# Kernel optimization log

Measured on AMD Instinct MI355X. Metric: run time of the kernel, lower is better.

## Reference

```python
import jax, jax.numpy as jnp
import numpy as np

B, N, S, K, D = 4, 8192, 2048, 32, 64
RADIUS = 0.2
MLP = [64, 64, 128]
C_IN = 3 + D  # 67
EPS = 1e-5  # BatchNorm eps


def setup_inputs() -> dict:
    key = jax.random.key(0)
    ks = jax.random.split(key, 8)
    inp = {
        "xyz": jax.random.uniform(ks[0], (B, N, 3), dtype=jnp.float32),
        "points": jax.random.normal(ks[1], (B, N, D), dtype=jnp.float32) * 0.1,
    }
    c = C_IN
    for i, o in enumerate(MLP):
        inp[f"w{i}"] = jax.random.normal(ks[2 + i], (o, c), dtype=jnp.float32) / np.sqrt(c).astype(np.float32)
        inp[f"b{i}"] = jnp.zeros((o,), jnp.float32)
        inp[f"g{i}"] = jnp.ones((o,), jnp.float32)
        inp[f"be{i}"] = jnp.zeros((o,), jnp.float32)
        c = o
    return inp


def _farthest_point_sample(xyz, npoint):
    # xyz: [B,N,3] -> idx [B,npoint]. Deterministic start at index 0
    # (torch version uses a random start index).
    Bb, Nn, _ = xyz.shape

    def step(carry, _):
        dist, far = carry
        centroid = jnp.take_along_axis(xyz, far[:, None, None], axis=1)  # [B,1,3]
        d = jnp.sum((xyz - centroid) ** 2, axis=-1)  # [B,N]
        dist = jnp.minimum(dist, d)
        nxt = jnp.argmax(dist, axis=-1).astype(jnp.int32)
        return (dist, nxt), far

    init = (jnp.full((Bb, Nn), 1e18, xyz.dtype), jnp.zeros((Bb,), jnp.int32))
    _, idx = jax.lax.scan(step, init, None, length=npoint)  # [npoint,B]
    return idx.T


def _square_distance(src, dst):
    # src [B,S,3], dst [B,N,3] -> [B,S,N]
    d = -2.0 * jnp.einsum("bsc,bnc->bsn", src, dst)
    d = d + jnp.sum(src ** 2, -1)[:, :, None] + jnp.sum(dst ** 2, -1)[:, None, :]
    return jnp.maximum(d, 0.0)


def _query_ball_point(radius, nsample, xyz, new_xyz):
    Bb, Nn, _ = xyz.shape
    sqr = _square_distance(new_xyz, xyz)  # [B,S,N]
    gi = jnp.broadcast_to(jnp.arange(Nn, dtype=jnp.int32), sqr.shape)
    gi = jnp.where(sqr > radius ** 2, Nn, gi)
    gi = jnp.sort(gi, axis=-1)[..., :nsample]  # [B,S,nsample]
    first = gi[..., :1]
    gi = jnp.where(gi >= Nn, first, gi)
    return jnp.clip(gi, 0, Nn - 1)


def _forward(xyz, points, params):
    bidx = jnp.arange(B)[:, None]
    fps_idx = _farthest_point_sample(xyz, S)          # [B,S]
    new_xyz = xyz[bidx, fps_idx]                      # [B,S,3]
    idx = _query_ball_point(RADIUS, K, xyz, new_xyz)  # [B,S,K]
    bidx3 = jnp.arange(B)[:, None, None]
    grouped_xyz = xyz[bidx3, idx]                     # [B,S,K,3]
    gnorm = grouped_xyz - new_xyz[:, :, None, :]
    gpts = points[bidx3, idx]                         # [B,S,K,D]
    feat = jnp.concatenate([gnorm, gpts], axis=-1)    # [B,S,K,3+D]
    x = jnp.transpose(feat, (0, 3, 2, 1))             # [B,C,K,S]
    for (w, b, g, be) in params:
        x = jnp.einsum("oc,bcks->boks", w, x) + b[None, :, None, None]
        mu = jnp.mean(x, axis=(0, 2, 3), keepdims=True)     # BN training mode
        var = jnp.var(x, axis=(0, 2, 3), keepdims=True)
        x = g[None, :, None, None] * (x - mu) * jax.lax.rsqrt(var + EPS) + be[None, :, None, None]
        x = jax.nn.relu(x)
    new_points = jnp.max(x, axis=2)                   # [B,mlp[-1],S]
    return new_xyz, new_points


def reference(xyz, points, w0, b0, g0, be0, w1, b1, g1, be1, w2, b2, g2, be2):
    params = ((w0, b0, g0, be0), (w1, b1, g1, be1), (w2, b2, g2, be2))
    return _forward(xyz, points, params)
```

## Files before the change

### kernel.cpp

```cpp
#include <hip/hip_runtime.h>
#include <hip/hip_bf16.h>

#define BB 4
#define NN 8192
#define SS 2048
#define KK 32
#define DD 64
#define CIN 67
#define PPIX (BB*SS*KK)
#define CNT_F 262144.0f
#define R2 0.04f
#define BN_EPS 1e-5f

typedef unsigned long long ull;

__global__ void zero_kernel(float* __restrict__ p, int n) {
    int i = blockIdx.x * 256 + threadIdx.x;
    if (i < n) p[i] = 0.0f;
}

__global__ __launch_bounds__(512) void fps_kernel(const float* __restrict__ xyz,
                                                  float* __restrict__ out_newxyz) {
    const int b = blockIdx.x;
    const int t = threadIdx.x;
    const int w = t >> 6, lane = t & 63;
    const float* X = xyz + (size_t)b * NN * 3;

    float px[16], py[16], pz[16], dist[16];
#pragma unroll
    for (int j = 0; j < 16; j++) {
        int i = t * 16 + j;
        px[j] = X[3 * i];
        py[j] = X[3 * i + 1];
        pz[j] = X[3 * i + 2];
        dist[j] = 1e18f;
    }

    __shared__ ull sSlot[2][8];

    float cx = X[0], cy = X[1], cz = X[2];

    for (int s = 0; s < SS; s++) {
        if (t == 0) {
            float* o = out_newxyz + (size_t)(b * SS + s) * 3;
            o[0] = cx; o[1] = cy; o[2] = cz;
        }
        float bd = 0.0f; int bj = 0;
#pragma unroll
        for (int j = 0; j < 16; j++) {
            float dx = __fsub_rn(px[j], cx);
            float dy = __fsub_rn(py[j], cy);
            float dz = __fsub_rn(pz[j], cz);
            float d = __fadd_rn(__fadd_rn(__fmul_rn(dx, dx), __fmul_rn(dy, dy)),
                                __fmul_rn(dz, dz));
            float nd = fminf(dist[j], d);
            dist[j] = nd;
            if (nd > bd) { bd = nd; bj = j; }
        }
        float wm = bd;
#pragma unroll
        for (int off = 32; off; off >>= 1)
            wm = fmaxf(wm, __shfl_xor(wm, off, 64));
        ull eqmask = __ballot(bd == wm);
        if (lane == __ffsll(eqmask) - 1) {
            sSlot[s & 1][w] =
                ((ull)__float_as_uint(bd) << 32) | (unsigned)(NN - 1 - (t * 16 + bj));
        }
        __syncthreads();
        ull m = sSlot[s & 1][0];
#pragma unroll
        for (int i = 1; i < 8; i++) { ull v = sSlot[s & 1][i]; if (v > m) m = v; }
        int far = NN - 1 - (int)(m & 0xffffffffu);
        cx = X[3 * far]; cy = X[3 * far + 1]; cz = X[3 * far + 2];
    }
}

__global__ __launch_bounds__(256) void ball_kernel(const float* __restrict__ xyz,
                                                   const float* __restrict__ newxyz,
                                                   int* __restrict__ idx_out) {
    const int wave = threadIdx.x >> 6;
    const int lane = threadIdx.x & 63;
    const int q = blockIdx.x * 4 + wave;
    const int b = q >> 11;
    const float* X = xyz + (size_t)b * NN * 3;

    float sx = newxyz[(size_t)q * 3 + 0];
    float sy = newxyz[(size_t)q * 3 + 1];
    float sz = newxyz[(size_t)q * 3 + 2];
    float ssum = __fadd_rn(__fadd_rn(__fmul_rn(sx, sx), __fmul_rn(sy, sy)),
                           __fmul_rn(sz, sz));

    __shared__ int sIdx[4][32];
    int* my = sIdx[wave];

    int have = 0;
    for (int base = 0; base < NN && have < KK; base += 64) {
        int i = base + lane;
        float x = X[3 * i], y = X[3 * i + 1], z = X[3 * i + 2];
        float xsum = __fadd_rn(__fadd_rn(__fmul_rn(x, x), __fmul_rn(y, y)),
                               __fmul_rn(z, z));
        float dot = __fadd_rn(__fadd_rn(__fmul_rn(sx, x), __fmul_rn(sy, y)),
                              __fmul_rn(sz, z));
        float d = __fadd_rn(__fadd_rn(__fmul_rn(-2.0f, dot), ssum), xsum);
        d = fmaxf(d, 0.0f);
        bool in = (d <= R2);
        ull mask = __ballot(in);
        int pre = __popcll(mask & ((1ull << lane) - 1ull));
        if (in && (have + pre) < KK) my[have + pre] = i;
        have += __popcll(mask);
    }
    __syncthreads();
    if (lane < KK) {
        int v = (lane < have) ? my[lane] : my[0];
        idx_out[(size_t)q * KK + lane] = v;
    }
}

#define ACC_C(NOUT4, cc, f)                                                        \
    {                                                                              \
        const float4* wr = (const float4*)(&wT[(cc) * (NOUT4) * 4]);               \
        _Pragma("unroll") for (int o4 = 0; o4 < (NOUT4); o4++) {                   \
            float4 wv = wr[o4];                                                    \
            acc[4 * o4 + 0] = fmaf(wv.x, (f), acc[4 * o4 + 0]);                    \
            acc[4 * o4 + 1] = fmaf(wv.y, (f), acc[4 * o4 + 1]);                    \
            acc[4 * o4 + 2] = fmaf(wv.z, (f), acc[4 * o4 + 2]);                    \
            acc[4 * o4 + 3] = fmaf(wv.w, (f), acc[4 * o4 + 3]);                    \
        }                                                                          \
    }

__global__ __launch_bounds__(256) void layer1_kernel(const float* __restrict__ xyz,
                                                     const float* __restrict__ points,
                                                     const float* __restrict__ newxyz,
                                                     const int* __restrict__ idx,
                                                     const float* __restrict__ w,
                                                     const float* __restrict__ bias,
                                                     float* __restrict__ y) {
    __shared__ __align__(16) float wT[CIN * 64];
    for (int i = threadIdx.x; i < CIN * 64; i += 256) {
        int o = i / CIN, c = i - o * CIN;
        wT[c * 64 + o] = w[i];
    }
    __syncthreads();

    const int p = blockIdx.x * 256 + threadIdx.x;
    const int b = p >> 16;
    const int sk = p & 65535;
    const int s = sk >> 5;
    const int pt = idx[p];

    const float* xr = xyz + ((size_t)b * NN + pt) * 3;
    const float* nr = newxyz + ((size_t)(b * SS + s)) * 3;
    float g0 = __fsub_rn(xr[0], nr[0]);
    float g1 = __fsub_rn(xr[1], nr[1]);
    float g2 = __fsub_rn(xr[2], nr[2]);

    float acc[64];
#pragma unroll
    for (int o = 0; o < 64; o++) acc[o] = bias[o];

    ACC_C(16, 0, g0);
    ACC_C(16, 1, g1);
    ACC_C(16, 2, g2);

    const float4* prow = (const float4*)(points + ((size_t)b * NN + pt) * DD);
#pragma unroll 4
    for (int c4 = 0; c4 < 16; c4++) {
        float4 f4 = prow[c4];
        ACC_C(16, 3 + 4 * c4 + 0, f4.x);
        ACC_C(16, 3 + 4 * c4 + 1, f4.y);
        ACC_C(16, 3 + 4 * c4 + 2, f4.z);
        ACC_C(16, 3 + 4 * c4 + 3, f4.w);
    }
#pragma unroll 8
    for (int o = 0; o < 64; o++) y[(size_t)o * PPIX + p] = acc[o];
}

__global__ __launch_bounds__(256) void layer_mid_kernel(const float* __restrict__ yin,
                                                        const float* __restrict__ cs,
                                                        const float* __restrict__ csh,
                                                        const float* __restrict__ w,
                                                        const float* __restrict__ bias,
                                                        float* __restrict__ yout) {
    __shared__ __align__(16) float wT[64 * 64];
    for (int i = threadIdx.x; i < 64 * 64; i += 256) {
        int o = i >> 6, c = i & 63;
        wT[c * 64 + o] = w[i];
    }
    __syncthreads();

    const int p = blockIdx.x * 256 + threadIdx.x;
    float acc[64];
#pragma unroll
    for (int o = 0; o < 64; o++) acc[o] = bias[o];

#pragma unroll 4
    for (int c = 0; c < 64; c++) {
        float f = fmaxf(fmaf(yin[(size_t)c * PPIX + p], cs[c], csh[c]), 0.0f);
        ACC_C(16, c, f);
    }
#pragma unroll 8
    for (int o = 0; o < 64; o++) yout[(size_t)o * PPIX + p] = acc[o];
}

__global__ __launch_bounds__(256) void stats_kernel(const float* __restrict__ y,
                                                    float* __restrict__ sums) {
    const int c = blockIdx.x >> 5;
    const int chunk = blockIdx.x & 31;
    const float4* src = (const float4*)(y + (size_t)c * PPIX + (size_t)chunk * 8192);
    float s1 = 0.f, s2 = 0.f;
#pragma unroll
    for (int it = 0; it < 8; it++) {
        float4 v = src[(it << 8) + threadIdx.x];
        s1 += v.x + v.y + v.z + v.w;
        s2 = fmaf(v.x, v.x, s2);
        s2 = fmaf(v.y, v.y, s2);
        s2 = fmaf(v.z, v.z, s2);
        s2 = fmaf(v.w, v.w, s2);
    }
#pragma unroll
    for (int off = 32; off; off >>= 1) {
        s1 += __shfl_down(s1, off, 64);
        s2 += __shfl_down(s2, off, 64);
    }
    __shared__ float p1[4], p2[4];
    int wv = threadIdx.x >> 6;
    if ((threadIdx.x & 63) == 0) { p1[wv] = s1; p2[wv] = s2; }
    __syncthreads();
    if (threadIdx.x == 0) {
        atomicAdd(&sums[2 * c], p1[0] + p1[1] + p1[2] + p1[3]);
        atomicAdd(&sums[2 * c + 1], p2[0] + p2[1] + p2[2] + p2[3]);
    }
}

__global__ void coef_kernel(const float* __restrict__ sums,
                            const float* __restrict__ g,
                            const float* __restrict__ be,
                            float* __restrict__ coefOut, int C) {
    int c = threadIdx.x;
    if (c >= C) return;
    float mu = sums[2 * c] * (1.0f / CNT_F);
    float ex2 = sums[2 * c + 1] * (1.0f / CNT_F);
    float var = fmaxf(ex2 - mu * mu, 0.0f);
    float sc = g[c] / sqrtf(var + BN_EPS);
    coefOut[c] = sc;
    coefOut[C + c] = be[c] - mu * sc;
}

__global__ __launch_bounds__(256) void final_kernel(const float* __restrict__ y3,
                                                    const float* __restrict__ coef,
                                                    float* __restrict__ outp) {
    const int gid = blockIdx.x * 256 + threadIdx.x;
    const int s = gid & 2047;
    const int o = (gid >> 11) & 127;
    const int b = gid >> 18;
    const float sc = coef[o], sh = coef[128 + o];
    const float4* row = (const float4*)(y3 + (size_t)o * PPIX + ((size_t)(b * SS + s)) * KK);
    float m = 0.0f;
#pragma unroll
    for (int i = 0; i < 8; i++) {
        float4 v = row[i];
        m = fmaxf(m, fmaf(v.x, sc, sh));
        m = fmaxf(m, fmaf(v.y, sc, sh));
        m = fmaxf(m, fmaf(v.z, sc, sh));
        m = fmaxf(m, fmaf(v.w, sc, sh));
    }
    outp[gid] = m;
}

extern "C" void kernel_launch(void* const* d_in, const int* in_sizes, int n_in,
                              void* d_out, int out_size, void* d_ws, size_t ws_size,
                              hipStream_t stream) {
    const float* xyz = (const float*)d_in[0];
    const float* points = (const float*)d_in[1];
    const float* w0 = (const float*)d_in[2];
    const float* b0 = (const float*)d_in[3];
    const float* g0 = (const float*)d_in[4];
    const float* be0 = (const float*)d_in[5];
    const float* w1 = (const float*)d_in[6];
    const float* b1 = (const float*)d_in[7];
    const float* g1 = (const float*)d_in[8];
    const float* be1 = (const float*)d_in[9];
    const float* w2 = (const float*)d_in[10];
    const float* b2 = (const float*)d_in[11];
    const float* g2 = (const float*)d_in[12];
    const float* be2 = (const float*)d_in[13];
    float* out = (float*)d_out;

    char* ws = (char*)d_ws;
    int* ballIdx = (int*)(ws + (32 << 10));
    float* sums = (float*)(ws + (1 << 20) + (256 << 10));
    float* coef = sums + 768;
    float* y2 = (float*)(ws + (2ull << 20));
    float* y1 = (float*)(ws + (66ull << 20));
    float* y3 = (float*)(ws + (66ull << 20));

    zero_kernel<<<3, 256, 0, stream>>>(sums, 768);

    fps_kernel<<<BB, 512, 0, stream>>>(xyz, out);
    ball_kernel<<<(BB * SS) / 4, 256, 0, stream>>>(xyz, out, ballIdx);

    layer1_kernel<<<PPIX / 256, 256, 0, stream>>>(xyz, points, out, ballIdx, w0, b0, y1);
    stats_kernel<<<64 * 32, 256, 0, stream>>>(y1, sums + 0);
    coef_kernel<<<1, 64, 0, stream>>>(sums + 0, g0, be0, coef + 0, 64);

    layer_mid_kernel<<<PPIX / 256, 256, 0, stream>>>(y1, coef + 0, coef + 64, w1, b1, y2);
    stats_kernel<<<64 * 32, 256, 0, stream>>>(y2, sums + 256);
    coef_kernel<<<1, 64, 0, stream>>>(sums + 256, g1, be1, coef + 256, 64);

    layer_mid_kernel<<<PPIX / 256, 256, 0, stream>>>(y2, coef + 256, coef + 320,
                                                     w2, b2, y3);
    layer_mid_kernel<<<PPIX / 256, 256, 0, stream>>>(y2, coef + 256, coef + 320,
                                                     w2 + 64 * 64, b2 + 64,
                                                     y3 + (size_t)64 * PPIX);
    stats_kernel<<<128 * 32, 256, 0, stream>>>(y3, sums + 512);
    coef_kernel<<<1, 128, 0, stream>>>(sums + 512, g2, be2, coef + 512, 128);

    final_kernel<<<(BB * 128 * SS) / 256, 256, 0, stream>>>(y3, coef + 512, out + BB * SS * 3);
}
```

Measured before the change: 2.859 ms.

## Fuse BatchNorm statistics into MLP layer kernels and streamline FPS argmax

Removes the separate stats kernels by having each layer kernel reduce per-channel sum and sum-of-squares of its outputs through wave shuffles, shared-memory atomics and global atomics, so the large activation tensors no longer have to be re-read from memory. FPS now keeps its per-thread arrays as scalar registers, finds the thread maximum with fmaxf, recovers the winning index only in the elected lane, and passes the winning coordinates through shared memory instead of reloading them from global memory. The risks are extra shuffle work and register pressure in the layer kernels, and a different floating-point summation order for the statistics.

```diff
diff --git a/kernel.cpp b/kernel.cpp
--- a/kernel.cpp
+++ b/kernel.cpp
@@ -19,24 +19,28 @@
     if (i < n) p[i] = 0.0f;
 }
 
-__global__ __launch_bounds__(512) void fps_kernel(const float* __restrict__ xyz,
-                                                  float* __restrict__ out_newxyz) {
+__global__ __launch_bounds__(512, 2) void fps_kernel(const float* __restrict__ xyz,
+                                                     float* __restrict__ out_newxyz) {
     const int b = blockIdx.x;
     const int t = threadIdx.x;
     const int w = t >> 6, lane = t & 63;
     const float* X = xyz + (size_t)b * NN * 3;
 
-    float px[16], py[16], pz[16], dist[16];
-#pragma unroll
-    for (int j = 0; j < 16; j++) {
-        int i = t * 16 + j;
-        px[j] = X[3 * i];
-        py[j] = X[3 * i + 1];
-        pz[j] = X[3 * i + 2];
-        dist[j] = 1e18f;
-    }
-
-    __shared__ ull sSlot[2][8];
+#define FPS_DECL(J) float px##J, py##J, pz##J, ds##J;
+    FPS_DECL(0) FPS_DECL(1) FPS_DECL(2) FPS_DECL(3)
+    FPS_DECL(4) FPS_DECL(5) FPS_DECL(6) FPS_DECL(7)
+    FPS_DECL(8) FPS_DECL(9) FPS_DECL(10) FPS_DECL(11)
+    FPS_DECL(12) FPS_DECL(13) FPS_DECL(14) FPS_DECL(15)
+
+#define FPS_LOAD(J) { const int i = t * 16 + J; \
+    px##J = X[3*i]; py##J = X[3*i+1]; pz##J = X[3*i+2]; ds##J = 1e18f; }
+    FPS_LOAD(0) FPS_LOAD(1) FPS_LOAD(2) FPS_LOAD(3)
+    FPS_LOAD(4) FPS_LOAD(5) FPS_LOAD(6) FPS_LOAD(7)
+    FPS_LOAD(8) FPS_LOAD(9) FPS_LOAD(10) FPS_LOAD(11)
+    FPS_LOAD(12) FPS_LOAD(13) FPS_LOAD(14) FPS_LOAD(15)
+
+    __shared__ ull sKey[2][8];
+    __shared__ float sCx[2][8], sCy[2][8], sCz[2][8];
 
     float cx = X[0], cy = X[1], cz = X[2];
 
@@ -45,33 +49,46 @@
             float* o = out_newxyz + (size_t)(b * SS + s) * 3;
             o[0] = cx; o[1] = cy; o[2] = cz;
         }
-        float bd = 0.0f; int bj = 0;
-#pragma unroll
-        for (int j = 0; j < 16; j++) {
-            float dx = __fsub_rn(px[j], cx);
-            float dy = __fsub_rn(py[j], cy);
-            float dz = __fsub_rn(pz[j], cz);
-            float d = __fadd_rn(__fadd_rn(__fmul_rn(dx, dx), __fmul_rn(dy, dy)),
-                                __fmul_rn(dz, dz));
-            float nd = fminf(dist[j], d);
-            dist[j] = nd;
-            if (nd > bd) { bd = nd; bj = j; }
-        }
+        float bd = 0.0f;
+#define FPS_UPD(J) { \
+    float dx = __fsub_rn(px##J, cx); \
+    float dy = __fsub_rn(py##J, cy); \
+    float dz = __fsub_rn(pz##J, cz); \
+    float dd = __fadd_rn(__fadd_rn(__fmul_rn(dx, dx), __fmul_rn(dy, dy)), \
+                         __fmul_rn(dz, dz)); \
+    ds##J = fminf(ds##J, dd); \
+    bd = fmaxf(bd, ds##J); }
+        FPS_UPD(0) FPS_UPD(1) FPS_UPD(2) FPS_UPD(3)
+        FPS_UPD(4) FPS_UPD(5) FPS_UPD(6) FPS_UPD(7)
+        FPS_UPD(8) FPS_UPD(9) FPS_UPD(10) FPS_UPD(11)
+        FPS_UPD(12) FPS_UPD(13) FPS_UPD(14) FPS_UPD(15)
+
         float wm = bd;
 #pragma unroll
         for (int off = 32; off; off >>= 1)
             wm = fmaxf(wm, __shfl_xor(wm, off, 64));
-        ull eqmask = __ballot(bd == wm);
-        if (lane == __ffsll(eqmask) - 1) {
-            sSlot[s & 1][w] =
-                ((ull)__float_as_uint(bd) << 32) | (unsigned)(NN - 1 - (t * 16 + bj));
+        ull eq = __ballot(bd == wm);
+        if (lane == __ffsll(eq) - 1) {
+            int bj = 0;
+            float wx = px0, wy = py0, wz = pz0;
+#define FPS_PICK(J) if (ds##J == bd) { bj = J; wx = px##J; wy = py##J; wz = pz##J; }
+            FPS_PICK(15) FPS_PICK(14) FPS_PICK(13) FPS_PICK(12)
+            FPS_PICK(11) FPS_PICK(10) FPS_PICK(9) FPS_PICK(8)
+            FPS_PICK(7) FPS_PICK(6) FPS_PICK(5) FPS_PICK(4)
+            FPS_PICK(3) FPS_PICK(2) FPS_PICK(1) FPS_PICK(0)
+            sKey[s & 1][w] = ((ull)__float_as_uint(bd) << 32)
+                           | (unsigned)(NN - 1 - (t * 16 + bj));
+            sCx[s & 1][w] = wx; sCy[s & 1][w] = wy; sCz[s & 1][w] = wz;
         }
         __syncthreads();
-        ull m = sSlot[s & 1][0];
-#pragma unroll
-        for (int i = 1; i < 8; i++) { ull v = sSlot[s & 1][i]; if (v > m) m = v; }
-        int far = NN - 1 - (int)(m & 0xffffffffu);
-        cx = X[3 * far]; cy = X[3 * far + 1]; cz = X[3 * far + 2];
+        const int par = s & 1;
+        ull m = sKey[par][0]; int im = 0;
+#pragma unroll
+        for (int i = 1; i < 8; i++) {
+            ull v = sKey[par][i];
+            if (v > m) { m = v; im = i; }
+        }
+        cx = sCx[par][im]; cy = sCy[par][im]; cz = sCz[par][im];
     }
 }
 
@@ -116,6 +133,30 @@
     }
 }
 
+#define STATS_REDUCE(sumsPtr)                                                      \
+    {                                                                              \
+        __shared__ float sS[128];                                                  \
+        if (threadIdx.x < 128) sS[threadIdx.x] = 0.0f;                             \
+        __syncthreads();                                                           \
+        _Pragma("unroll") for (int o = 0; o < 64; o++) {                           \
+            float s1 = acc[o];                                                     \
+            float s2 = __fmul_rn(s1, s1);                                          \
+            _Pragma("unroll") for (int off = 32; off; off >>= 1) {                 \
+                s1 += __shfl_down(s1, off, 64);                                    \
+                s2 += __shfl_down(s2, off, 64);                                    \
+            }                                                                      \
+            if ((threadIdx.x & 63) == 0) {                                         \
+                atomicAdd(&sS[o], s1);                                             \
+                atomicAdd(&sS[64 + o], s2);                                        \
+            }                                                                      \
+        }                                                                          \
+        __syncthreads();                                                           \
+        if (threadIdx.x < 64)                                                      \
+            atomicAdd(&(sumsPtr)[2 * threadIdx.x], sS[threadIdx.x]);               \
+        else if (threadIdx.x < 128)                                                \
+            atomicAdd(&(sumsPtr)[2 * (threadIdx.x - 64) + 1], sS[threadIdx.x]);    \
+    }
+
 #define ACC_C(NOUT4, cc, f)                                                        \
     {                                                                              \
         const float4* wr = (const float4*)(&wT[(cc) * (NOUT4) * 4]);               \
@@ -134,7 +175,8 @@
                                                      const int* __restrict__ idx,
                                                      const float* __restrict__ w,
                                                      const float* __restrict__ bias,
-                                                     float* __restrict__ y) {
+                                                     float* __restrict__ y,
+                                                     float* __restrict__ sums) {
     __shared__ __align__(16) float wT[CIN * 64];
     for (int i = threadIdx.x; i < CIN * 64; i += 256) {
         int o = i / CIN, c = i - o * CIN;
@@ -173,6 +215,8 @@
     }
 #pragma unroll 8
     for (int o = 0; o < 64; o++) y[(size_t)o * PPIX + p] = acc[o];
+
+    STATS_REDUCE(sums);
 }
 
 __global__ __launch_bounds__(256) void layer_mid_kernel(const float* __restrict__ yin,
@@ -180,7 +224,8 @@
                                                         const float* __restrict__ csh,
                                                         const float* __restrict__ w,
                                                         const float* __restrict__ bias,
-                                                        float* __restrict__ yout) {
+                                                        float* __restrict__ yout,
+                                                        float* __restrict__ sums) {
     __shared__ __align__(16) float wT[64 * 64];
     for (int i = threadIdx.x; i < 64 * 64; i += 256) {
         int o = i >> 6, c = i & 63;
@@ -200,36 +245,8 @@
     }
 #pragma unroll 8
     for (int o = 0; o < 64; o++) yout[(size_t)o * PPIX + p] = acc[o];
-}
-
-__global__ __launch_bounds__(256) void stats_kernel(const float* __restrict__ y,
-                                                    float* __restrict__ sums) {
-    const int c = blockIdx.x >> 5;
-    const int chunk = blockIdx.x & 31;
-    const float4* src = (const float4*)(y + (size_t)c * PPIX + (size_t)chunk * 8192);
-    float s1 = 0.f, s2 = 0.f;
-#pragma unroll
-    for (int it = 0; it < 8; it++) {
-        float4 v = src[(it << 8) + threadIdx.x];
-        s1 += v.x + v.y + v.z + v.w;
-        s2 = fmaf(v.x, v.x, s2);
-        s2 = fmaf(v.y, v.y, s2);
-        s2 = fmaf(v.z, v.z, s2);
-        s2 = fmaf(v.w, v.w, s2);
-    }
-#pragma unroll
-    for (int off = 32; off; off >>= 1) {
-        s1 += __shfl_down(s1, off, 64);
-        s2 += __shfl_down(s2, off, 64);
-    }
-    __shared__ float p1[4], p2[4];
-    int wv = threadIdx.x >> 6;
-    if ((threadIdx.x & 63) == 0) { p1[wv] = s1; p2[wv] = s2; }
-    __syncthreads();
-    if (threadIdx.x == 0) {
-        atomicAdd(&sums[2 * c], p1[0] + p1[1] + p1[2] + p1[3]);
-        atomicAdd(&sums[2 * c + 1], p2[0] + p2[1] + p2[2] + p2[3]);
-    }
+
+    STATS_REDUCE(sums);
 }
 
 __global__ void coef_kernel(const float* __restrict__ sums,
@@ -299,20 +316,20 @@
     fps_kernel<<<BB, 512, 0, stream>>>(xyz, out);
     ball_kernel<<<(BB * SS) / 4, 256, 0, stream>>>(xyz, out, ballIdx);
 
-    layer1_kernel<<<PPIX / 256, 256, 0, stream>>>(xyz, points, out, ballIdx, w0, b0, y1);
-    stats_kernel<<<64 * 32, 256, 0, stream>>>(y1, sums + 0);
+    layer1_kernel<<<PPIX / 256, 256, 0, stream>>>(xyz, points, out, ballIdx, w0, b0,
+                                                  y1, sums + 0);
     coef_kernel<<<1, 64, 0, stream>>>(sums + 0, g0, be0, coef + 0, 64);
 
-    layer_mid_kernel<<<PPIX / 256, 256, 0, stream>>>(y1, coef + 0, coef + 64, w1, b1, y2);
-    stats_kernel<<<64 * 32, 256, 0, stream>>>(y2, sums + 256);
+    layer_mid_kernel<<<PPIX / 256, 256, 0, stream>>>(y1, coef + 0, coef + 64, w1, b1,
+                                                     y2, sums + 256);
     coef_kernel<<<1, 64, 0, stream>>>(sums + 256, g1, be1, coef + 256, 64);
 
     layer_mid_kernel<<<PPIX / 256, 256, 0, stream>>>(y2, coef + 256, coef + 320,
-                                                     w2, b2, y3);
+                                                     w2, b2, y3, sums + 512);
     layer_mid_kernel<<<PPIX / 256, 256, 0, stream>>>(y2, coef + 256, coef + 320,
                                                      w2 + 64 * 64, b2 + 64,
-                                                     y3 + (size_t)64 * PPIX);
-    stats_kernel<<<128 * 32, 256, 0, stream>>>(y3, sums + 512);
+                                                     y3 + (size_t)64 * PPIX,
+                                                     sums + 512 + 128);
     coef_kernel<<<1, 128, 0, stream>>>(sums + 512, g2, be2, coef + 512, 128);
 
     final_kernel<<<(BB * 128 * SS) / 256, 256, 0, stream>>>(y3, coef + 512, out + BB * SS * 3);
```

New measurement: 3.508 ms. 22.7% more time.

## Stage FPS points in LDS and reduce with packed 64-bit keys over four waves

Applied to the files above, without the earlier changes.

The farthest-point-sampling kernel now copies each batch's points into shared memory once. The next centroid is read from LDS instead of global memory on every one of the serial iterations. The block shrinks from 512 to 256 threads, each owning 32 strided points. The cross-lane argmax becomes a single 64-bit shuffle-max on a packed (distance, reversed index) key instead of a float max, ballot and store, and only four wave results are merged after the barrier. The aim is to shorten the latency of each serial step, at the cost of re-reading point coordinates from LDS every iteration instead of keeping them in registers.

```diff
diff --git a/kernel.cpp b/kernel.cpp
--- a/kernel.cpp
+++ b/kernel.cpp
@@ -19,26 +19,34 @@
     if (i < n) p[i] = 0.0f;
 }
 
-__global__ __launch_bounds__(512) void fps_kernel(const float* __restrict__ xyz,
-                                                  float* __restrict__ out_newxyz) {
+#define FPS_ALL(M) M(0) M(1) M(2) M(3) M(4) M(5) M(6) M(7) \
+                   M(8) M(9) M(10) M(11) M(12) M(13) M(14) M(15) \
+                   M(16) M(17) M(18) M(19) M(20) M(21) M(22) M(23) \
+                   M(24) M(25) M(26) M(27) M(28) M(29) M(30) M(31)
+
+__global__ __launch_bounds__(256, 1) void fps_kernel(const float* __restrict__ xyz,
+                                                     float* __restrict__ out_newxyz) {
     const int b = blockIdx.x;
     const int t = threadIdx.x;
-    const int w = t >> 6, lane = t & 63;
+    const int w = t >> 6;
     const float* X = xyz + (size_t)b * NN * 3;
 
-    float px[16], py[16], pz[16], dist[16];
-#pragma unroll
-    for (int j = 0; j < 16; j++) {
-        int i = t * 16 + j;
-        px[j] = X[3 * i];
-        py[j] = X[3 * i + 1];
-        pz[j] = X[3 * i + 2];
-        dist[j] = 1e18f;
-    }
-
-    __shared__ ull sSlot[2][8];
-
-    float cx = X[0], cy = X[1], cz = X[2];
+    __shared__ float2 sXY[NN];
+    __shared__ float  sZ[NN];
+    __shared__ ull    sKey[2][4];
+
+    for (int i = t; i < NN; i += 256) {
+        sXY[i] = make_float2(X[3 * i], X[3 * i + 1]);
+        sZ[i] = X[3 * i + 2];
+    }
+    __syncthreads();
+
+#define FPS_FD(J) float d##J = 1e18f;
+    FPS_ALL(FPS_FD)
+
+    const int base_comp = (NN - 1) - t;
+
+    float cx = sXY[0].x, cy = sXY[0].y, cz = sZ[0];
 
     for (int s = 0; s < SS; s++) {
         if (t == 0) {
@@ -46,32 +54,35 @@
             o[0] = cx; o[1] = cy; o[2] = cz;
         }
         float bd = 0.0f; int bj = 0;
-#pragma unroll
-        for (int j = 0; j < 16; j++) {
-            float dx = __fsub_rn(px[j], cx);
-            float dy = __fsub_rn(py[j], cy);
-            float dz = __fsub_rn(pz[j], cz);
-            float d = __fadd_rn(__fadd_rn(__fmul_rn(dx, dx), __fmul_rn(dy, dy)),
-                                __fmul_rn(dz, dz));
-            float nd = fminf(dist[j], d);
-            dist[j] = nd;
-            if (nd > bd) { bd = nd; bj = j; }
+#define FPS_UPD(J) { \
+        float2 v = sXY[(J << 8) + t]; \
+        float zz = sZ[(J << 8) + t]; \
+        float dx = __fsub_rn(v.x, cx); \
+        float dy = __fsub_rn(v.y, cy); \
+        float dz = __fsub_rn(zz, cz); \
+        float dd = __fadd_rn(__fadd_rn(__fmul_rn(dx, dx), __fmul_rn(dy, dy)), \
+                             __fmul_rn(dz, dz)); \
+        d##J = fminf(d##J, dd); \
+        if (d##J > bd) { bd = d##J; bj = J; } }
+        FPS_ALL(FPS_UPD)
+
+        ull key = ((ull)__float_as_uint(bd) << 13)
+                | (unsigned)(base_comp - (bj << 8));
+#pragma unroll
+        for (int off = 32; off; off >>= 1) {
+            ull o = __shfl_xor(key, off, 64);
+            if (o > key) key = o;
         }
-        float wm = bd;
-#pragma unroll
-        for (int off = 32; off; off >>= 1)
-            wm = fmaxf(wm, __shfl_xor(wm, off, 64));
-        ull eqmask = __ballot(bd == wm);
-        if (lane == __ffsll(eqmask) - 1) {
-            sSlot[s & 1][w] =
-                ((ull)__float_as_uint(bd) << 32) | (unsigned)(NN - 1 - (t * 16 + bj));
-        }
+        if ((t & 63) == 0) sKey[s & 1][w] = key;
         __syncthreads();
-        ull m = sSlot[s & 1][0];
-#pragma unroll
-        for (int i = 1; i < 8; i++) { ull v = sSlot[s & 1][i]; if (v > m) m = v; }
-        int far = NN - 1 - (int)(m & 0xffffffffu);
-        cx = X[3 * far]; cy = X[3 * far + 1]; cz = X[3 * far + 2];
+        const int par = s & 1;
+        ull m = sKey[par][0];
+        { ull v1 = sKey[par][1]; if (v1 > m) m = v1; }
+        { ull v2 = sKey[par][2]; if (v2 > m) m = v2; }
+        { ull v3 = sKey[par][3]; if (v3 > m) m = v3; }
+        const int idx = (NN - 1) - (int)(m & 0x1FFF);
+        float2 c2 = sXY[idx];
+        cx = c2.x; cy = c2.y; cz = sZ[idx];
     }
 }
 
@@ -296,7 +307,7 @@
 
     zero_kernel<<<3, 256, 0, stream>>>(sums, 768);
 
-    fps_kernel<<<BB, 512, 0, stream>>>(xyz, out);
+    fps_kernel<<<BB, 256, 0, stream>>>(xyz, out);
     ball_kernel<<<(BB * SS) / 4, 256, 0, stream>>>(xyz, out, ballIdx);
 
     layer1_kernel<<<PPIX / 256, 256, 0, stream>>>(xyz, points, out, ballIdx, w0, b0, y1);
```

New measurement: 3.657 ms. 1.28x slower.
